# Performance work log

Measured on AMD Instinct MI355X. Metric: run time of the kernel, lower is better.

Reference implementation:

```python
import jax, jax.numpy as jnp
import numpy as np

N_NODES = 100000
N_EDGES = 1200000
NUM_GRAPHS = 128
IN_DIM = 5
HIDDEN = 64


def setup_inputs() -> dict:
    key = jax.random.key(0)
    ks = jax.random.split(key, 12)
    x = jax.random.normal(ks[0], (N_NODES, IN_DIM), dtype=jnp.float32)
    edge_index = jax.random.randint(ks[1], (2, N_EDGES), 0, N_NODES, dtype=jnp.int64 if jax.config.read('jax_enable_x64') else jnp.int32)
    batch = jnp.sort(jax.random.randint(ks[2], (N_NODES,), 0, NUM_GRAPHS, dtype=jnp.int32))
    s = lambda fan_in: 1.0 / np.sqrt(fan_in)
    return {
        'x': x,
        'edge_index': edge_index,
        'batch': batch,
        'w_rel1': jax.random.normal(ks[3], (IN_DIM, HIDDEN), dtype=jnp.float32) * s(IN_DIM),
        'b_rel1': jnp.zeros((HIDDEN,), dtype=jnp.float32),
        'w_root1': jax.random.normal(ks[4], (IN_DIM, HIDDEN), dtype=jnp.float32) * s(IN_DIM),
        'w_rel2': jax.random.normal(ks[5], (HIDDEN, HIDDEN), dtype=jnp.float32) * s(HIDDEN),
        'b_rel2': jnp.zeros((HIDDEN,), dtype=jnp.float32),
        'w_root2': jax.random.normal(ks[6], (HIDDEN, HIDDEN), dtype=jnp.float32) * s(HIDDEN),
        'w_h1': jax.random.normal(ks[7], (2 * HIDDEN, HIDDEN), dtype=jnp.float32) * s(2 * HIDDEN),
        'b_h1': jnp.zeros((HIDDEN,), dtype=jnp.float32),
        'w_h2': jax.random.normal(ks[8], (HIDDEN, 1), dtype=jnp.float32) * s(HIDDEN),
        'b_h2': jnp.zeros((1,), dtype=jnp.float32),
    }


def _graph_conv(x, src, dst, w_rel, b_rel, w_root):
    # PyG GraphConv (aggr='add'): out = aggr(x_src -> dst) @ W_rel + b_rel + x @ W_root
    agg = jax.ops.segment_sum(x[src], dst, num_segments=N_NODES)
    return agg @ w_rel + b_rel + x @ w_root


def reference(x, edge_index, batch,
              w_rel1, b_rel1, w_root1,
              w_rel2, b_rel2, w_root2,
              w_h1, b_h1, w_h2, b_h2):
    src, dst = edge_index[0], edge_index[1]
    h = jax.nn.relu(_graph_conv(x, src, dst, w_rel1, b_rel1, w_root1))
    h = jax.nn.relu(_graph_conv(h, src, dst, w_rel2, b_rel2, w_root2))
    # global add + mean pooling over graphs
    add_pool = jax.ops.segment_sum(h, batch, num_segments=NUM_GRAPHS)
    counts = jax.ops.segment_sum(jnp.ones((N_NODES,), h.dtype), batch, num_segments=NUM_GRAPHS)
    mean_pool = add_pool / jnp.maximum(counts, 1.0)[:, None]
    g = jnp.concatenate([mean_pool, add_pool], axis=1)  # [G, 2*HIDDEN]
    out = jax.nn.relu(g @ w_h1 + b_h1) @ w_h2 + b_h2
    return out.squeeze(-1)
```

## Files before the change

kernel.cpp:

```cpp
#include <hip/hip_runtime.h>
#include <hip/hip_bf16.h>

#define N_NODES    100000
#define N_EDGES    1200000
#define NUM_GRAPHS 128
#define IN_DIM     5
#define HIDDEN     64
#define M_TILES    (N_NODES / 16)
#define NI4        (N_EDGES / 4)

#define CB    782
#define CBLK  256
#define EPB   ((NI4 + CBLK - 1) / CBLK)

typedef __attribute__((ext_vector_type(8))) short short8;
typedef __attribute__((ext_vector_type(4))) float f32x4;
typedef __attribute__((ext_vector_type(2))) float f32x2;

#if defined(__has_builtin)
#if __has_builtin(__builtin_amdgcn_cvt_pk_f32_fp8)
#define HAS_HWF8 1
#endif
#endif

__device__ __forceinline__ unsigned short f2bs(float f) {
    union { float f; unsigned u; } v; v.f = f;
    return (unsigned short)((v.u + 0x7FFFu + ((v.u >> 16) & 1u)) >> 16);
}
__device__ __forceinline__ float bs2f(unsigned short s) {
    union { unsigned u; float f; } v; v.u = ((unsigned)s) << 16;
    return v.f;
}
__device__ __forceinline__ float blo(unsigned p) { return bs2f((unsigned short)(p & 0xffff)); }
__device__ __forceinline__ float bhi(unsigned p) { return bs2f((unsigned short)(p >> 16)); }
__device__ __forceinline__ unsigned pack2(float a, float b) {
    return ((unsigned)f2bs(b) << 16) | (unsigned)f2bs(a);
}

__device__ __forceinline__ unsigned char f2f8(float f) {
    union { float f; unsigned u; } v; v.f = f * 0x1p-120f;
    unsigned u = v.u + 0x7FFFFu + ((v.u >> 20) & 1u);
    return (unsigned char)(u >> 20);
}
__device__ __forceinline__ float f82f(unsigned b) {
    union { unsigned u; float f; } v; v.u = (b & 0x7Fu) << 20;
    return v.f * 0x1p120f;
}

__device__ __forceinline__ void acc8(float4& a, unsigned r) {
#ifdef HAS_HWF8
    f32x2 lo = __builtin_amdgcn_cvt_pk_f32_fp8((int)r, false);
    f32x2 hi = __builtin_amdgcn_cvt_pk_f32_fp8((int)r, true);
    a.x += lo[0]; a.y += lo[1]; a.z += hi[0]; a.w += hi[1];
#else
    a.x += f82f(r); a.y += f82f(r >> 8); a.z += f82f(r >> 16); a.w += f82f(r >> 24);
#endif
}


__global__ void coarse_count(const int* __restrict__ dst, int* __restrict__ gcnt,
                             const float* __restrict__ x, uint4* __restrict__ xb,
                             float* __restrict__ add_pool, int* __restrict__ ptr) {
    __shared__ int h[CB];
    int t = threadIdx.x, b = blockIdx.x;
    for (int i = t; i < CB; i += 256) h[i] = 0;
    __syncthreads();
    int i0 = b * EPB, i1 = min(i0 + EPB, NI4);
    for (int i = i0 + t; i < i1; i += 256) {
        int4 d = ((const int4*)dst)[i];
        atomicAdd(&h[d.x >> 7], 1);
        atomicAdd(&h[d.y >> 7], 1);
        atomicAdd(&h[d.z >> 7], 1);
        atomicAdd(&h[d.w >> 7], 1);
    }
    __syncthreads();
    for (int i = t; i < CB; i += 256) gcnt[b * CB + i] = h[i];

    for (int n = b * 256 + t; n < N_NODES; n += CBLK * 256) {
        const float* xr = x + (size_t)n * IN_DIM;
        uint4 o;
        o.x = pack2(xr[0], xr[1]);
        o.y = pack2(xr[2], xr[3]);
        o.z = pack2(xr[4], 0.0f);
        o.w = 0u;
        xb[n] = o;
    }
    if (b == 0) {
        for (int i = t; i < NUM_GRAPHS * HIDDEN; i += 256) add_pool[i] = 0.0f;
        if (t == 0) ptr[N_NODES] = N_EDGES;
    }
}

__global__ void partition_k(const int* __restrict__ src, const int* __restrict__ dst,
                            const int* __restrict__ gcnt, int* __restrict__ bstart,
                            int* __restrict__ part) {
    __shared__ int sp[CB];
    __shared__ int st[CB];
    __shared__ int h[CB];
    int t = threadIdx.x, b = blockIdx.x;

    for (int k = t; k < CB; k += 256) {
        int pref = 0, tot = 0;
        for (int bp = 0; bp < CBLK; ++bp) {
            int v = gcnt[bp * CB + k];
            tot += v;
            if (bp < b) pref += v;
        }
        sp[k] = pref;
        st[k] = tot;
        h[k] = 0;
    }
    __syncthreads();

    if (t < 64) {
        int loc[13];
        int base_i = t * 13;
        int sum = 0;
#pragma unroll
        for (int j = 0; j < 13; ++j) {
            int idx = base_i + j;
            int c = (idx < CB) ? st[idx] : 0;
            loc[j] = sum; sum += c;
        }
        int inc = sum;
#pragma unroll
        for (int off = 1; off < 64; off <<= 1) {
            int u = __shfl_up(inc, off, 64);
            if (t >= off) inc += u;
        }
        int excl = inc - sum;
#pragma unroll
        for (int j = 0; j < 13; ++j) {
            int idx = base_i + j;
            if (idx < CB) st[idx] = excl + loc[j];
        }
    }
    __syncthreads();

    for (int k = t; k < CB; k += 256) {
        int bs = st[k];
        sp[k] = bs + sp[k];
        if (b == 0) bstart[k] = bs;
    }
    if (b == 0 && t == 0) bstart[CB] = N_EDGES;
    __syncthreads();

    int i0 = b * EPB, i1 = min(i0 + EPB, NI4);
    for (int i = i0 + t; i < i1; i += 256) {
        int4 s4 = ((const int4*)src)[i];
        int4 d4 = ((const int4*)dst)[i];
        int k, r;
        k = d4.x >> 7; r = atomicAdd(&h[k], 1); part[sp[k] + r] = s4.x | ((d4.x & 127) << 17);
        k = d4.y >> 7; r = atomicAdd(&h[k], 1); part[sp[k] + r] = s4.y | ((d4.y & 127) << 17);
        k = d4.z >> 7; r = atomicAdd(&h[k], 1); part[sp[k] + r] = s4.z | ((d4.z & 127) << 17);
        k = d4.w >> 7; r = atomicAdd(&h[k], 1); part[sp[k] + r] = s4.w | ((d4.w & 127) << 17);
    }
}

__global__ void fine_gather1(const int* __restrict__ part, const int* __restrict__ bstart,
                             int* __restrict__ ptr, int* __restrict__ esrc,
                             const uint4* __restrict__ xb,
                             const float* __restrict__ x,
                             const float* __restrict__ w_rel1,
                             const float* __restrict__ b_rel1,
                             const float* __restrict__ w_root1,
                             unsigned short* __restrict__ h1,
                             unsigned char* __restrict__ h1f8) {
    __shared__ int fh[128];
    __shared__ int fo[128];
    __shared__ int fr[128];
    int k = blockIdx.x, t = threadIdx.x;
    int e0 = bstart[k], e1 = bstart[k + 1];
    if (t < 128) { fh[t] = 0; fr[t] = 0; }
    __syncthreads();
    for (int e = e0 + t; e < e1; e += 256)
        atomicAdd(&fh[(part[e] >> 17) & 127], 1);
    __syncthreads();
    int v = (t < 128) ? fh[t] : 0;
    if (t < 128) fo[t] = v;
    __syncthreads();
    for (int off = 1; off < 128; off <<= 1) {
        int u = (t >= off && t < 128) ? fo[t - off] : 0;
        __syncthreads();
        if (t < 128) fo[t] += u;
        __syncthreads();
    }
    if (t < 128) {
        int excl = fo[t] - v;
        int n_t = (k << 7) + t;
        if (n_t < N_NODES) ptr[n_t] = e0 + excl;
        fh[t] = excl;
    }
    __syncthreads();
    for (int e = e0 + t; e < e1; e += 256) {
        int p = part[e];
        int d = (p >> 17) & 127;
        int r = atomicAdd(&fr[d], 1);
        esrc[e0 + fh[d] + r] = p & 0x1FFFF;
    }
    __syncthreads();

    int ql = t & 15;
    int g  = t >> 4;
    float wr[IN_DIM][4], wo[IN_DIM][4], bias[4];
#pragma unroll
    for (int j = 0; j < 4; ++j) {
        int ch = ql * 4 + j;
        bias[j] = b_rel1[ch];
#pragma unroll
        for (int kk = 0; kk < IN_DIM; ++kk) {
            wr[kk][j] = w_rel1[kk * HIDDEN + ch];
            wo[kk][j] = w_root1[kk * HIDDEN + ch];
        }
    }

    for (int nl = g; nl < 128; nl += 16) {
        int n = (k << 7) + nl;
        if (n >= N_NODES) break;
        int start = e0 + fh[nl];
        int end   = (nl < 127) ? (e0 + fh[nl + 1]) : e1;
        float a[IN_DIM] = {0.f, 0.f, 0.f, 0.f, 0.f};
        for (int e = start + ql; e < end; e += 16) {
            uint4 p = xb[esrc[e]];
            a[0] += blo(p.x); a[1] += bhi(p.x);
            a[2] += blo(p.y); a[3] += bhi(p.y);
            a[4] += blo(p.z);
        }
#pragma unroll
        for (int kk = 0; kk < IN_DIM; ++kk) {
            a[kk] += __shfl_xor(a[kk], 1, 64);
            a[kk] += __shfl_xor(a[kk], 2, 64);
            a[kk] += __shfl_xor(a[kk], 4, 64);
            a[kk] += __shfl_xor(a[kk], 8, 64);
        }
        float xr[IN_DIM];
#pragma unroll
        for (int kk = 0; kk < IN_DIM; ++kk) xr[kk] = x[(size_t)n * IN_DIM + kk];

        unsigned short hv[4];
        unsigned char  hf[4];
#pragma unroll
        for (int j = 0; j < 4; ++j) {
            float acc = bias[j];
#pragma unroll
            for (int kk = 0; kk < IN_DIM; ++kk)
                acc += a[kk] * wr[kk][j] + xr[kk] * wo[kk][j];
            float h = fmaxf(acc, 0.0f);
            hv[j] = f2bs(h);
            hf[j] = f2f8(h);
        }
        ushort4 v4; v4.x = hv[0]; v4.y = hv[1]; v4.z = hv[2]; v4.w = hv[3];
        *(ushort4*)(h1 + (size_t)n * HIDDEN + ql * 4) = v4;
        uchar4 c4; c4.x = hf[0]; c4.y = hf[1]; c4.z = hf[2]; c4.w = hf[3];
        *(uchar4*)(h1f8 + (size_t)n * HIDDEN + ql * 4) = c4;
    }
}


__global__ void gather2_fp8(const unsigned* __restrict__ rows,
                            const int* __restrict__ ptr,
                            const int* __restrict__ esrc,
                            uint2* __restrict__ agg2) {
    int t    = threadIdx.x;
    int ql   = t & 15;
    int grp  = (blockIdx.x * blockDim.x + t) >> 4;
    int ngrp = (gridDim.x * blockDim.x) >> 4;

    for (int n = grp; n < N_NODES; n += ngrp) {
        int start = ptr[n], end = ptr[n + 1];
        float4 a0 = {0.f,0.f,0.f,0.f}, a1 = a0, a2 = a0, a3 = a0;
        int e = start;
        for (; e + 3 < end; e += 4) {
            int s0 = esrc[e], s1 = esrc[e + 1], s2 = esrc[e + 2], s3 = esrc[e + 3];
            unsigned r0 = rows[(size_t)s0 * 16 + ql];
            unsigned r1 = rows[(size_t)s1 * 16 + ql];
            unsigned r2 = rows[(size_t)s2 * 16 + ql];
            unsigned r3 = rows[(size_t)s3 * 16 + ql];
            acc8(a0, r0); acc8(a1, r1); acc8(a2, r2); acc8(a3, r3);
        }
        for (; e < end; ++e) {
            unsigned r0 = rows[(size_t)esrc[e] * 16 + ql];
            acc8(a0, r0);
        }
        float4 a;
        a.x = (a0.x + a1.x) + (a2.x + a3.x);
        a.y = (a0.y + a1.y) + (a2.y + a3.y);
        a.z = (a0.z + a1.z) + (a2.z + a3.z);
        a.w = (a0.w + a1.w) + (a2.w + a3.w);
        uint2 o;
        o.x = pack2(a.x, a.y);
        o.y = pack2(a.z, a.w);
        agg2[(size_t)n * 16 + ql] = o;
    }
}

__global__ void mlp2_pool(const unsigned short* __restrict__ agg2,
                          const unsigned short* __restrict__ h1,
                          const float* __restrict__ w_rel2,
                          const float* __restrict__ b_rel2,
                          const float* __restrict__ w_root2,
                          const int* __restrict__ batch,
                          float* __restrict__ add_pool) {
    int lane = threadIdx.x & 63;
    int wv   = threadIdx.x >> 6;
    int row  = lane & 15;
    int quad = lane >> 4;
    int n    = wv * 16 + row;

    short8 bwr[2], bwo[2];
#pragma unroll
    for (int s = 0; s < 2; ++s)
#pragma unroll
        for (int j = 0; j < 8; ++j) {
            int k = 32 * s + quad * 8 + j;
            bwr[s][j] = (short)f2bs(w_rel2[k * HIDDEN + n]);
            bwo[s][j] = (short)f2bs(w_root2[k * HIDDEN + n]);
        }
    float bias = b_rel2[n];

    for (int t = blockIdx.x; t < M_TILES; t += gridDim.x) {
        int m0 = t * 16;
        size_t rbase = (size_t)(m0 + row) * HIDDEN;
        short8 aa0 = *(const short8*)(agg2 + rbase + quad * 8);
        short8 aa1 = *(const short8*)(agg2 + rbase + 32 + quad * 8);
        short8 ah0 = *(const short8*)(h1   + rbase + quad * 8);
        short8 ah1 = *(const short8*)(h1   + rbase + 32 + quad * 8);

        f32x4 acc = {bias, bias, bias, bias};
        acc = __builtin_amdgcn_mfma_f32_16x16x32_bf16(aa0, bwr[0], acc, 0, 0, 0);
        acc = __builtin_amdgcn_mfma_f32_16x16x32_bf16(aa1, bwr[1], acc, 0, 0, 0);
        acc = __builtin_amdgcn_mfma_f32_16x16x32_bf16(ah0, bwo[0], acc, 0, 0, 0);
        acc = __builtin_amdgcn_mfma_f32_16x16x32_bf16(ah1, bwo[1], acc, 0, 0, 0);

        float hv0 = fmaxf(acc[0], 0.0f), hv1 = fmaxf(acc[1], 0.0f);
        float hv2 = fmaxf(acc[2], 0.0f), hv3 = fmaxf(acc[3], 0.0f);

        int gLo = batch[m0], gHi = batch[m0 + 15];
        if (gLo == gHi) {
            float s = (hv0 + hv1) + (hv2 + hv3);
            s += __shfl_xor(s, 16, 64);
            s += __shfl_xor(s, 32, 64);
            if (quad == 0)
                atomicAdd(&add_pool[gLo * HIDDEN + n], s);
        } else {
            int m = m0 + quad * 4;
            atomicAdd(&add_pool[batch[m]     * HIDDEN + n], hv0);
            atomicAdd(&add_pool[batch[m + 1] * HIDDEN + n], hv1);
            atomicAdd(&add_pool[batch[m + 2] * HIDDEN + n], hv2);
            atomicAdd(&add_pool[batch[m + 3] * HIDDEN + n], hv3);
        }
    }
}

__device__ __forceinline__ int lower_bound_i(const int* a, int n, int v) {
    int lo = 0, hi = n;
    while (lo < hi) { int mid = (lo + hi) >> 1; if (a[mid] < v) lo = mid + 1; else hi = mid; }
    return lo;
}

__global__ void head_mlp(const float* __restrict__ add_pool,
                         const int* __restrict__ batch,
                         const float* __restrict__ w_h1,
                         const float* __restrict__ b_h1,
                         const float* __restrict__ w_h2,
                         const float* __restrict__ b_h2,
                         float* __restrict__ out) {
    int g = blockIdx.x, t = threadIdx.x;

    __shared__ int s_cnt;
    if (t == 0) {
        int start = lower_bound_i(batch, N_NODES, g);
        int end   = lower_bound_i(batch, N_NODES, g + 1);
        s_cnt = end - start;
    }
    __syncthreads();
    float cnt = fmaxf((float)s_cnt, 1.0f);

    __shared__ float sg[2 * HIDDEN];
    float add = add_pool[(size_t)g * HIDDEN + t];
    sg[t]          = add / cnt;
    sg[HIDDEN + t] = add;
    __syncthreads();

    float hid = b_h1[t];
#pragma unroll 16
    for (int i = 0; i < 2 * HIDDEN; ++i)
        hid += sg[i] * w_h1[i * HIDDEN + t];
    hid = fmaxf(hid, 0.0f);

    float res = hid * w_h2[t];
    for (int off = 32; off > 0; off >>= 1)
        res += __shfl_down(res, off, 64);
    if (t == 0) out[g] = res + b_h2[0];
}

extern "C" void kernel_launch(void* const* d_in, const int* in_sizes, int n_in,
                              void* d_out, int out_size, void* d_ws, size_t ws_size,
                              hipStream_t stream) {
    const float* x       = (const float*)d_in[0];
    const int*   ei      = (const int*)d_in[1];
    const int*   src     = ei;
    const int*   dst     = ei + N_EDGES;
    const int*   batch   = (const int*)d_in[2];
    const float* w_rel1  = (const float*)d_in[3];
    const float* b_rel1  = (const float*)d_in[4];
    const float* w_root1 = (const float*)d_in[5];
    const float* w_rel2  = (const float*)d_in[6];
    const float* b_rel2  = (const float*)d_in[7];
    const float* w_root2 = (const float*)d_in[8];
    const float* w_h1    = (const float*)d_in[9];
    const float* b_h1    = (const float*)d_in[10];
    const float* w_h2    = (const float*)d_in[11];
    const float* b_h2    = (const float*)d_in[12];
    float* out = (float*)d_out;

    int* base = (int*)d_ws;
    int*   gcnt     = base;
    int*   bstart   = gcnt + ((CBLK * CB + 3) & ~3);
    float* add_pool = (float*)(bstart + ((CB + 1 + 3) & ~3));
    int*   ptr      = (int*)(add_pool + NUM_GRAPHS * HIDDEN);
    int*   part     = ptr + ((N_NODES + 1 + 3) & ~3);
    int*   esrc     = part + N_EDGES;
    unsigned short* h1   = (unsigned short*)(esrc + N_EDGES);
    unsigned short* agg2 = h1 + (size_t)N_NODES * HIDDEN;
    unsigned char*  h1f8 = (unsigned char*)(agg2 + (size_t)N_NODES * HIDDEN);
    uint4*          xb   = (uint4*)(h1f8 + (size_t)N_NODES * HIDDEN);

    coarse_count<<<CBLK, 256, 0, stream>>>(dst, gcnt, x, xb, add_pool, ptr);
    partition_k<<<CBLK, 256, 0, stream>>>(src, dst, gcnt, bstart, part);

    fine_gather1<<<CB, 256, 0, stream>>>(part, bstart, ptr, esrc, xb, x,
                                         w_rel1, b_rel1, w_root1, h1, h1f8);
    gather2_fp8<<<2048, 256, 0, stream>>>((const unsigned*)h1f8, ptr, esrc, (uint2*)agg2);
    mlp2_pool<<<2048, 256, 0, stream>>>(agg2, h1, w_rel2, b_rel2, w_root2, batch, add_pool);
    head_mlp<<<NUM_GRAPHS, 64, 0, stream>>>(add_pool, batch, w_h1, b_h1, w_h2, b_h2, out);
}
```

Baseline: 227.9 us.

## Move bucket prefix sums into dedicated scan kernels and stage gathered features in LDS

The per-block redundant prefix over all 256 coarse-count blocks inside partition_k is replaced by two separate scan kernels: a per-bucket scan across blocks and a single-block scan over bucket totals. partition_k then just loads precomputed offsets. This removes each block's O(CBLK*CB) global read loop. Separately, fine_gather1 copies the gathered xb rows into a 48KB LDS stage during the edge-sort pass and later aggregates from LDS instead of re-gathering from global memory. The cost is two extra kernel launches and more LDS per block, which may lower occupancy.

```diff
diff --git a/kernel.cpp b/kernel.cpp
--- a/kernel.cpp
+++ b/kernel.cpp
@@ -12,6 +12,7 @@
 #define CB    782
 #define CBLK  256
 #define EPB   ((NI4 + CBLK - 1) / CBLK)
+#define STCAP 3072
 
 typedef __attribute__((ext_vector_type(8))) short short8;
 typedef __attribute__((ext_vector_type(4))) float f32x4;
@@ -91,69 +92,58 @@
     }
 }
 
+__global__ void block_scan(int* __restrict__ gcnt, int* __restrict__ btot) {
+    __shared__ int s[CBLK];
+    int k = blockIdx.x, t = threadIdx.x;
+    int v = gcnt[t * CB + k];
+    s[t] = v;
+    __syncthreads();
+    for (int off = 1; off < CBLK; off <<= 1) {
+        int u = (t >= off) ? s[t - off] : 0;
+        __syncthreads();
+        s[t] += u;
+        __syncthreads();
+    }
+    gcnt[t * CB + k] = s[t] - v;
+    if (t == CBLK - 1) btot[k] = s[t];
+}
+
+__global__ void bucket_scan(const int* __restrict__ btot, int* __restrict__ bstart) {
+    __shared__ int s[1024];
+    int t = threadIdx.x;
+    int v = (t < CB) ? btot[t] : 0;
+    s[t] = v;
+    __syncthreads();
+    for (int off = 1; off < 1024; off <<= 1) {
+        int u = (t >= off) ? s[t - off] : 0;
+        __syncthreads();
+        s[t] += u;
+        __syncthreads();
+    }
+    if (t < CB) bstart[t] = s[t] - v;
+    if (t == 0) bstart[CB] = N_EDGES;
+}
+
 __global__ void partition_k(const int* __restrict__ src, const int* __restrict__ dst,
-                            const int* __restrict__ gcnt, int* __restrict__ bstart,
+                            const int* __restrict__ gcnt, const int* __restrict__ bstart,
                             int* __restrict__ part) {
-    __shared__ int sp[CB];
-    __shared__ int st[CB];
+    __shared__ int base[CB];
     __shared__ int h[CB];
     int t = threadIdx.x, b = blockIdx.x;
-
-    for (int k = t; k < CB; k += 256) {
-        int pref = 0, tot = 0;
-        for (int bp = 0; bp < CBLK; ++bp) {
-            int v = gcnt[bp * CB + k];
-            tot += v;
-            if (bp < b) pref += v;
-        }
-        sp[k] = pref;
-        st[k] = tot;
-        h[k] = 0;
-    }
-    __syncthreads();
-
-    if (t < 64) {
-        int loc[13];
-        int base_i = t * 13;
-        int sum = 0;
-#pragma unroll
-        for (int j = 0; j < 13; ++j) {
-            int idx = base_i + j;
-            int c = (idx < CB) ? st[idx] : 0;
-            loc[j] = sum; sum += c;
-        }
-        int inc = sum;
-#pragma unroll
-        for (int off = 1; off < 64; off <<= 1) {
-            int u = __shfl_up(inc, off, 64);
-            if (t >= off) inc += u;
-        }
-        int excl = inc - sum;
-#pragma unroll
-        for (int j = 0; j < 13; ++j) {
-            int idx = base_i + j;
-            if (idx < CB) st[idx] = excl + loc[j];
-        }
-    }
-    __syncthreads();
-
-    for (int k = t; k < CB; k += 256) {
-        int bs = st[k];
-        sp[k] = bs + sp[k];
-        if (b == 0) bstart[k] = bs;
-    }
-    if (b == 0 && t == 0) bstart[CB] = N_EDGES;
-    __syncthreads();
-
+    for (int i = t; i < CB; i += 256) {
+        base[i] = bstart[i] + gcnt[b * CB + i];
+        h[i] = 0;
+    }
+    __syncthreads();
     int i0 = b * EPB, i1 = min(i0 + EPB, NI4);
     for (int i = i0 + t; i < i1; i += 256) {
         int4 s4 = ((const int4*)src)[i];
         int4 d4 = ((const int4*)dst)[i];
         int k, r;
-        k = d4.x >> 7; r = atomicAdd(&h[k], 1); part[sp[k] + r] = s4.x | ((d4.x & 127) << 17);
-        k = d4.y >> 7; r = atomicAdd(&h[k], 1); part[sp[k] + r] = s4.y | ((d4.y & 127) << 17);
-        k = d4.z >> 7; r = atomicAdd(&h[k], 1); part[sp[k] + r] = s4.z | ((d4.z & 127) << 17);
-        k = d4.w >> 7; r = atomicAdd(&h[k], 1); part[sp[k] + r] = s4.w | ((d4.w & 127) << 17);
+        k = d4.x >> 7; r = atomicAdd(&h[k], 1); part[base[k] + r] = s4.x | ((d4.x & 127) << 17);
+        k = d4.y >> 7; r = atomicAdd(&h[k], 1); part[base[k] + r] = s4.y | ((d4.y & 127) << 17);
+        k = d4.z >> 7; r = atomicAdd(&h[k], 1); part[base[k] + r] = s4.z | ((d4.z & 127) << 17);
+        k = d4.w >> 7; r = atomicAdd(&h[k], 1); part[base[k] + r] = s4.w | ((d4.w & 127) << 17);
     }
 }
 
@@ -169,8 +159,11 @@
     __shared__ int fh[128];
     __shared__ int fo[128];
     __shared__ int fr[128];
+    __shared__ uint4 stage[STCAP];
     int k = blockIdx.x, t = threadIdx.x;
     int e0 = bstart[k], e1 = bstart[k + 1];
+    int ne = e1 - e0;
+    bool useLds = (ne <= STCAP);
     if (t < 128) { fh[t] = 0; fr[t] = 0; }
     __syncthreads();
     for (int e = e0 + t; e < e1; e += 256)
@@ -195,8 +188,11 @@
     for (int e = e0 + t; e < e1; e += 256) {
         int p = part[e];
         int d = (p >> 17) & 127;
+        int s = p & 0x1FFFF;
         int r = atomicAdd(&fr[d], 1);
-        esrc[e0 + fh[d] + r] = p & 0x1FFFF;
+        int slot = fh[d] + r;
+        esrc[e0 + slot] = s;
+        if (useLds) stage[slot] = xb[s];
     }
     __syncthreads();
 
@@ -217,14 +213,23 @@
     for (int nl = g; nl < 128; nl += 16) {
         int n = (k << 7) + nl;
         if (n >= N_NODES) break;
-        int start = e0 + fh[nl];
-        int end   = (nl < 127) ? (e0 + fh[nl + 1]) : e1;
+        int s0 = fh[nl];
+        int s1 = (nl < 127) ? fh[nl + 1] : ne;
         float a[IN_DIM] = {0.f, 0.f, 0.f, 0.f, 0.f};
-        for (int e = start + ql; e < end; e += 16) {
-            uint4 p = xb[esrc[e]];
-            a[0] += blo(p.x); a[1] += bhi(p.x);
-            a[2] += blo(p.y); a[3] += bhi(p.y);
-            a[4] += blo(p.z);
+        if (useLds) {
+            for (int i = s0 + ql; i < s1; i += 16) {
+                uint4 p = stage[i];
+                a[0] += blo(p.x); a[1] += bhi(p.x);
+                a[2] += blo(p.y); a[3] += bhi(p.y);
+                a[4] += blo(p.z);
+            }
+        } else {
+            for (int i = s0 + ql; i < s1; i += 16) {
+                uint4 p = xb[esrc[e0 + i]];
+                a[0] += blo(p.x); a[1] += bhi(p.x);
+                a[2] += blo(p.y); a[3] += bhi(p.y);
+                a[4] += blo(p.z);
+            }
         }
 #pragma unroll
         for (int kk = 0; kk < IN_DIM; ++kk) {
@@ -416,7 +421,8 @@
 
     int* base = (int*)d_ws;
     int*   gcnt     = base;
-    int*   bstart   = gcnt + ((CBLK * CB + 3) & ~3);
+    int*   btot     = gcnt + ((CBLK * CB + 3) & ~3);
+    int*   bstart   = btot + ((CB + 3) & ~3);
     float* add_pool = (float*)(bstart + ((CB + 1 + 3) & ~3));
     int*   ptr      = (int*)(add_pool + NUM_GRAPHS * HIDDEN);
     int*   part     = ptr + ((N_NODES + 1 + 3) & ~3);
@@ -427,6 +433,8 @@
     uint4*          xb   = (uint4*)(h1f8 + (size_t)N_NODES * HIDDEN);
 
     coarse_count<<<CBLK, 256, 0, stream>>>(dst, gcnt, x, xb, add_pool, ptr);
+    block_scan<<<CB, CBLK, 0, stream>>>(gcnt, btot);
+    bucket_scan<<<1, 1024, 0, stream>>>(btot, bstart);
     partition_k<<<CBLK, 256, 0, stream>>>(src, dst, gcnt, bstart, part);
 
     fine_gather1<<<CB, 256, 0, stream>>>(part, bstart, ptr, esrc, xb, x,
```

Result: faster. 195.4 us (-14.2%).
